# Optimization experiments

Hardware: AMD Instinct MI355X
Metric: run time of the kernel (lower is better)

## Reference

```python
import jax, jax.numpy as jnp
import numpy as np

# ---- dims (match init_kwargs) ----
D_MODEL = 512
N_HEADS = 8
EXPAND = 2
SHRINK = 1
BATCH = 8
SEQ = 4096            # == tno_max_l
DPB_DIM = 512         # dpb_embedding
D1 = EXPAND * D_MODEL                 # 1024 (u_proj / o1 out)
D2 = D_MODEL // SHRINK                # 512  (v_proj out)
HEAD_DIM = D2 // N_HEADS              # 64
EPS = 1e-8


def _srms(x, d):
    # SimpleRMSNorm: x / (||x||_2 * d^-0.5 + eps)
    norm = jnp.linalg.norm(x, axis=-1, keepdims=True)
    return x / (norm * (d ** -0.5) + EPS)


def _dpb(p, Wp, bp, W1, b1, W2, b2, W3, b3):
    # dynamic position bias MLP: scalar rel-pos -> h*head_dim kernel coeffs
    x = p @ Wp + bp
    x = jax.nn.relu(_srms(x, DPB_DIM)) @ W1 + b1
    x = jax.nn.relu(_srms(x, DPB_DIM)) @ W2 + b2
    x = jax.nn.relu(_srms(x, DPB_DIM)) @ W3 + b3
    return x  # (m, h*head_dim)


def _heads(k):
    # (m, h*d) -> (h, m, d)
    return k.reshape(-1, N_HEADS, HEAD_DIM).transpose(1, 0, 2)


def setup_inputs() -> dict:
    key = jax.random.key(0)
    ks = jax.random.split(key, 17)
    w = lambda k, shape: jax.random.normal(k, shape, dtype=jnp.float32) * 0.02
    return {
        "x": jax.random.normal(ks[0], (BATCH, SEQ, D_MODEL), dtype=jnp.float32),
        "Wu": w(ks[1], (D_MODEL, D1)), "bu": w(ks[2], (D1,)),
        "Wv": w(ks[3], (D_MODEL, D2)), "bv": w(ks[4], (D2,)),
        "Wo1": w(ks[5], (D2, D1)), "bo1": w(ks[6], (D1,)),
        "Wo2": w(ks[7], (D1, D_MODEL)), "bo2": w(ks[8], (D_MODEL,)),
        "dpb_Wp": w(ks[9], (1, DPB_DIM)), "dpb_bp": w(ks[10], (DPB_DIM,)),
        "dpb_W1": w(ks[11], (DPB_DIM, DPB_DIM)), "dpb_b1": w(ks[12], (DPB_DIM,)),
        "dpb_W2": w(ks[13], (DPB_DIM, DPB_DIM)), "dpb_b2": w(ks[14], (DPB_DIM,)),
        "dpb_W3": w(ks[15], (DPB_DIM, N_HEADS * HEAD_DIM)),
        "dpb_b3": w(ks[16], (N_HEADS * HEAD_DIM,)),
    }


def reference(x, Wu, bu, Wv, bv, Wo1, bo1, Wo2, bo2,
              dpb_Wp, dpb_bp, dpb_W1, dpb_b1, dpb_W2, dpb_b2, dpb_W3, dpb_b3):
    b, n, _ = x.shape
    shortcut = x
    xn = _srms(x, D2)                                  # pre_norm (SimpleRMSNorm(d2))
    u = jax.nn.silu(xn @ Wu + bu)                      # (b, n, d1)
    v = jax.nn.silu(xn @ Wv + bv)                      # (b, n, d2)
    v = v.reshape(b, n, N_HEADS, HEAD_DIM).transpose(0, 2, 1, 3)  # (b, h, n, d)

    # relative-position indices (par_type=1): 1..n-1, -(n-1)..-1, 0
    pos_idx = jnp.arange(1, n, dtype=jnp.float32)[:, None]   # (n-1, 1)
    neg_idx = -pos_idx[::-1]                                  # (n-1, 1)
    zero_idx = jnp.zeros((1, 1), jnp.float32)
    dpb = lambda p: _dpb(p, dpb_Wp, dpb_bp, dpb_W1, dpb_b1,
                         dpb_W2, dpb_b2, dpb_W3, dpb_b3)
    kz = _heads(dpb(zero_idx))   # (h, 1,   d)
    kp = _heads(dpb(pos_idx))    # (h, n-1, d)
    kn = _heads(dpb(neg_idx))    # (h, n-1, d)
    # circulant embedding of the Toeplitz kernel: [t0, t1..t{n-1}, 0, t{-(n-1)}..t{-1}]
    a = jnp.concatenate([kz, kp, kz, kn], axis=1)             # (h, 2n, d)

    m = 2 * n
    yf = jnp.fft.rfft(v, m, axis=-2)                          # (b, h, n+1, d) complex
    af = jnp.fft.rfft(a, m, axis=-2)[None]                    # (1, h, n+1, d)
    out = jnp.fft.irfft(yf * af, m, axis=-2)[..., :n, :]      # (b, h, n, d)

    out = out.transpose(0, 2, 1, 3).reshape(b, n, D2)         # b n (h d)
    out = (out @ Wo1 + bo1) * u                               # gate
    out = out @ Wo2 + bo2 + shortcut
    return out
```

## Files before the change

### kernel.cpp

```cpp
#include <hip/hip_runtime.h>
#include <hip/hip_fp16.h>


#define FFTN 8192
#define SWZ(p) ((p) ^ (((p) >> 8) & 31))

#define C45F 0.70710678118654752f
#define CC8F 0.92387953251128676f
#define SS8F 0.38268343236508977f

typedef unsigned short u16;
typedef unsigned int u32;
typedef __attribute__((ext_vector_type(8))) short bf16x8;
typedef __attribute__((ext_vector_type(4))) float f32x4;

__device__ __forceinline__ int brev13(int x) { return (int)(__brev((unsigned)x) >> 19); }
__device__ __forceinline__ float b2f(u16 u) {
  union { float f; u32 i; } c; c.i = ((u32)u) << 16; return c.f;
}
__device__ __forceinline__ u16 f2b(float f) {
  union { float f; u32 i; } c; c.f = f;
  u32 r = c.i + 0x7FFFu + ((c.i >> 16) & 1u);
  return (u16)(r >> 16);
}
__device__ __forceinline__ float silu_f(float x) { return x / (1.f + __expf(-x)); }

__device__ __forceinline__ float2 up2(u32 v) {
  __half2 h = __builtin_bit_cast(__half2, v);
  return make_float2(__low2float(h), __high2float(h));
}
__device__ __forceinline__ u32 dn2(float r, float i) {
  __half2 h = __floats2half2_rn(r, i);
  return __builtin_bit_cast(u32, h);
}

__device__ __forceinline__ void gload16(const void* g, void* l) {
  __builtin_amdgcn_global_load_lds(
      (const __attribute__((address_space(1))) u32*)g,
      (__attribute__((address_space(3))) u32*)l, 16, 0, 0);
}

__global__ void twiddle_init_kernel(float2* __restrict__ tw) {
  int k = blockIdx.x * blockDim.x + threadIdx.x;
  if (k < 4096) {
    double ang = -6.283185307179586476925286766559 * ((double)k / 8192.0);
    tw[k] = make_float2((float)cos(ang), (float)sin(ang));
  }
}

__global__ __launch_bounds__(256) void srms_bf16_kernel(
    const float* __restrict__ in, u16* __restrict__ out, int rows, int do_relu)
{
  int wave = threadIdx.x >> 6, lane = threadIdx.x & 63;
  int row = (blockIdx.x << 2) + wave;
  if (row >= rows) return;
  const float4* p = (const float4*)(in + (size_t)row * 512);
  float4 a = p[lane], b = p[lane + 64];
  float ss = a.x*a.x + a.y*a.y + a.z*a.z + a.w*a.w
           + b.x*b.x + b.y*b.y + b.z*b.z + b.w*b.w;
#pragma unroll
  for (int off = 32; off > 0; off >>= 1) ss += __shfl_xor(ss, off);
  float inv = 1.0f / (sqrtf(ss) * 0.04419417382415922f + 1e-8f);
  a.x *= inv; a.y *= inv; a.z *= inv; a.w *= inv;
  b.x *= inv; b.y *= inv; b.z *= inv; b.w *= inv;
  if (do_relu) {
    a.x = fmaxf(a.x, 0.f); a.y = fmaxf(a.y, 0.f); a.z = fmaxf(a.z, 0.f); a.w = fmaxf(a.w, 0.f);
    b.x = fmaxf(b.x, 0.f); b.y = fmaxf(b.y, 0.f); b.z = fmaxf(b.z, 0.f); b.w = fmaxf(b.w, 0.f);
  }
  u16* o = out + (size_t)row * 512;
  ushort4 s0, s1;
  s0.x = f2b(a.x); s0.y = f2b(a.y); s0.z = f2b(a.z); s0.w = f2b(a.w);
  s1.x = f2b(b.x); s1.y = f2b(b.y); s1.z = f2b(b.z); s1.w = f2b(b.w);
  *(ushort4*)(o + lane * 4) = s0;
  *(ushort4*)(o + 256 + lane * 4) = s1;
}

__global__ __launch_bounds__(256) void dpb0_kernel(
    const float* __restrict__ Wp, const float* __restrict__ bp, u16* __restrict__ out)
{
  int wave = threadIdx.x >> 6, lane = threadIdx.x & 63;
  int row = (blockIdx.x << 2) + wave;
  if (row >= 8192) return;
  float pv;
  if (row == 0 || row == 4096) pv = 0.f;
  else if (row < 4096) pv = (float)row;
  else pv = (float)(row - 8192);
  const float4* wp  = (const float4*)Wp;
  const float4* bpp = (const float4*)bp;
  float4 a = wp[lane], b = wp[lane + 64];
  float4 c = bpp[lane], d = bpp[lane + 64];
  a.x = fmaf(pv, a.x, c.x); a.y = fmaf(pv, a.y, c.y);
  a.z = fmaf(pv, a.z, c.z); a.w = fmaf(pv, a.w, c.w);
  b.x = fmaf(pv, b.x, d.x); b.y = fmaf(pv, b.y, d.y);
  b.z = fmaf(pv, b.z, d.z); b.w = fmaf(pv, b.w, d.w);
  float ss = a.x*a.x + a.y*a.y + a.z*a.z + a.w*a.w
           + b.x*b.x + b.y*b.y + b.z*b.z + b.w*b.w;
#pragma unroll
  for (int off = 32; off > 0; off >>= 1) ss += __shfl_xor(ss, off);
  float inv = 1.0f / (sqrtf(ss) * 0.04419417382415922f + 1e-8f);
  u16* o = out + (size_t)row * 512;
  ushort4 s0, s1;
  s0.x = f2b(fmaxf(a.x * inv, 0.f)); s0.y = f2b(fmaxf(a.y * inv, 0.f));
  s0.z = f2b(fmaxf(a.z * inv, 0.f)); s0.w = f2b(fmaxf(a.w * inv, 0.f));
  s1.x = f2b(fmaxf(b.x * inv, 0.f)); s1.y = f2b(fmaxf(b.y * inv, 0.f));
  s1.z = f2b(fmaxf(b.z * inv, 0.f)); s1.w = f2b(fmaxf(b.w * inv, 0.f));
  *(ushort4*)(o + lane * 4) = s0;
  *(ushort4*)(o + 256 + lane * 4) = s1;
}

__global__ __launch_bounds__(256) void wtrans_kernel(
    const float* __restrict__ in, u16* __restrict__ out, int R, int C)
{
  __shared__ float tile[32][33];
  const int c0 = blockIdx.x << 5, r0 = blockIdx.y << 5;
  const int tx = threadIdx.x, ty = threadIdx.y;
#pragma unroll
  for (int i = 0; i < 32; i += 8)
    tile[ty + i][tx] = in[(size_t)(r0 + ty + i) * C + c0 + tx];
  __syncthreads();
#pragma unroll
  for (int i = 0; i < 32; i += 8)
    out[(size_t)(c0 + ty + i) * R + r0 + tx] = f2b(tile[tx][ty + i]);
}

__global__ __launch_bounds__(256) void transpose_b16_kernel(
    const u16* __restrict__ in, u16* __restrict__ out)
{
  __shared__ u16 tile[32][33];
  const int b = blockIdx.z;
  const int j0 = blockIdx.x << 5, c0 = blockIdx.y << 5;
  const int tx = threadIdx.x, ty = threadIdx.y;
  const u16* ip = in + ((size_t)b << 21);
  u16* op = out + ((size_t)b << 21);
#pragma unroll
  for (int i = 0; i < 32; i += 8)
    tile[ty + i][tx] = ip[(size_t)(c0 + ty + i) * 4096 + j0 + tx];
  __syncthreads();
#pragma unroll
  for (int i = 0; i < 32; i += 8)
    op[(size_t)(j0 + ty + i) * 512 + c0 + tx] = tile[tx][ty + i];
}

template <int EPI>
__global__ __launch_bounds__(256) void gemm_bf16_kernel(
    const u16* __restrict__ A, const u16* __restrict__ Bt,
    const float* __restrict__ bias, const u16* __restrict__ aux16,
    const float* __restrict__ auxf, void* __restrict__ Cv,
    int M, int N, int K)
{
  __shared__ __align__(16) u16 As[4096];
  __shared__ __align__(16) u16 Bs[4096];
  const int tid = threadIdx.x;
  const int lane = tid & 63;
  const int w = tid >> 6;
  const int wm = (w >> 1) << 6;
  const int wn = (w & 1) << 6;
  const int lm = lane & 15;
  const int lq = lane >> 4;
  const int bm = blockIdx.y << 7;
  const int bn = blockIdx.x << 7;

  const int sm = tid & 127;
  const int sk = tid >> 7;
  const u16* Ap = A + (size_t)(bm + sm) * K + sk * 8;
  const u16* Bp = Bt + (size_t)(bn + sm) * K + sk * 8;
  u16* As0 = As + ((sk)     * 128 + sm) * 8;
  u16* As1 = As + ((2 + sk) * 128 + sm) * 8;
  u16* Bs0 = Bs + ((sk)     * 128 + sm) * 8;
  u16* Bs1 = Bs + ((2 + sk) * 128 + sm) * 8;

  f32x4 acc[4][4];
#pragma unroll
  for (int i = 0; i < 4; i++)
#pragma unroll
    for (int j = 0; j < 4; j++) acc[i][j] = (f32x4){0.f, 0.f, 0.f, 0.f};

  for (int k0 = 0; k0 < K; k0 += 32) {
    __syncthreads();
    gload16(Ap, As0); gload16(Ap + 16, As1);
    gload16(Bp, Bs0); gload16(Bp + 16, Bs1);
    Ap += 32; Bp += 32;
    __builtin_amdgcn_s_waitcnt(0);
    __syncthreads();
    bf16x8 af[4], bfr[4];
#pragma unroll
    for (int i = 0; i < 4; i++) {
      af[i]  = *(const bf16x8*)(As + (lq * 128 + wm + i * 16 + lm) * 8);
      bfr[i] = *(const bf16x8*)(Bs + (lq * 128 + wn + i * 16 + lm) * 8);
    }
#pragma unroll
    for (int i = 0; i < 4; i++)
#pragma unroll
      for (int j = 0; j < 4; j++)
        acc[i][j] = __builtin_amdgcn_mfma_f32_16x16x32_bf16(af[i], bfr[j], acc[i][j], 0, 0, 0);
  }

#pragma unroll
  for (int i = 0; i < 4; i++) {
    const int m0 = bm + wm + i * 16 + lq * 4;
#pragma unroll
    for (int j = 0; j < 4; j++) {
      const int n = bn + wn + j * 16 + lm;
      const float bb = bias[n];
      const f32x4 v = acc[i][j];
      if constexpr (EPI == 2) {
        const int b = m0 >> 12;
        const int jq = m0 & 4095;
        ushort4 s;
        s.x = f2b(silu_f(v[0] + bb)); s.y = f2b(silu_f(v[1] + bb));
        s.z = f2b(silu_f(v[2] + bb)); s.w = f2b(silu_f(v[3] + bb));
        *(ushort4*)((u16*)Cv + (((size_t)(b * 512 + n)) << 12) + jq) = s;
      } else if constexpr (EPI == 5) {
        float4 o = make_float4(v[0] + bb, v[1] + bb, v[2] + bb, v[3] + bb);
        *(float4*)((float*)Cv + (size_t)n * M + m0) = o;
      } else {
#pragma unroll
        for (int r = 0; r < 4; r++) {
          const size_t idx = (size_t)(m0 + r) * N + n;
          const float val = v[r] + bb;
          if constexpr (EPI == 0) ((float*)Cv)[idx] = val;
          if constexpr (EPI == 1) ((u16*)Cv)[idx] = f2b(silu_f(val));
          if constexpr (EPI == 3) ((u16*)Cv)[idx] = f2b(val * b2f(aux16[idx]));
          if constexpr (EPI == 4) ((float*)Cv)[idx] = val + auxf[idx];
        }
      }
    }
  }
}

__device__ __forceinline__ void fft8192_dit(float* sr, float* si,
                                            const float2* __restrict__ tw)
{
  const int t = threadIdx.x;
  for (int s = 0; s < 12; s += 2) {
    __syncthreads();
    const int h = 1 << s;
#pragma unroll
    for (int bb = 0; bb < 4; bb++) {
      const int u = t + (bb << 9);
      const int j = u & (h - 1);
      const int base = ((u >> s) << (s + 2)) | j;
      const float2 w1 = tw[j << (12 - s)];
      const float2 w2 = tw[j << (11 - s)];
      const int q0 = SWZ(base), q1 = SWZ(base + h);
      const int q2 = SWZ(base + 2 * h), q3 = SWZ(base + 3 * h);
      const float ar = sr[q0], ai = si[q0];
      const float br = sr[q1], bi = si[q1];
      const float cr = sr[q2], ci = si[q2];
      const float dr = sr[q3], di = si[q3];
      const float t1r = br * w1.x - bi * w1.y, t1i = br * w1.y + bi * w1.x;
      const float t2r = dr * w1.x - di * w1.y, t2i = dr * w1.y + di * w1.x;
      const float Ar = ar + t1r, Ai = ai + t1i;
      const float Br = ar - t1r, Bi = ai - t1i;
      const float Cr = cr + t2r, Ci = ci + t2i;
      const float Dr = cr - t2r, Di = ci - t2i;
      const float t3r = Cr * w2.x - Ci * w2.y, t3i = Cr * w2.y + Ci * w2.x;
      const float pr  = Dr * w2.x - Di * w2.y, pi  = Dr * w2.y + Di * w2.x;
      const float t4r = pi, t4i = -pr;
      sr[q0] = Ar + t3r; si[q0] = Ai + t3i;
      sr[q2] = Ar - t3r; si[q2] = Ai - t3i;
      sr[q1] = Br + t4r; si[q1] = Bi + t4i;
      sr[q3] = Br - t4r; si[q3] = Bi - t4i;
    }
  }
  __syncthreads();
#pragma unroll
  for (int bb = 0; bb < 8; bb++) {
    const int u = t + (bb << 9);
    const float2 w = tw[u];
    const int p0 = SWZ(u), p1 = SWZ(u + 4096);
    const float br = sr[p1], bi = si[p1];
    const float trr = br * w.x - bi * w.y;
    const float tri = br * w.y + bi * w.x;
    const float ar = sr[p0], ai = si[p0];
    sr[p0] = ar + trr; si[p0] = ai + tri;
    sr[p1] = ar - trr; si[p1] = ai - tri;
  }
  __syncthreads();
}

__global__ __launch_bounds__(512) void kfft_kernel(
    const float* __restrict__ D1T,
    const float2* __restrict__ tw,
    float2* __restrict__ aspec)
{
  __shared__ float sr[FFTN];
  __shared__ float si[FFTN];
  const int q = blockIdx.x;
  const int t = threadIdx.x;
  const float* row0 = D1T + ((size_t)(2 * q)) * 8192;
  const float* row1 = row0 + 8192;
#pragma unroll
  for (int it = 0; it < 16; it++) {
    const int r = t + (it << 9);
    const int d = SWZ(brev13(r));
    sr[d] = row0[r]; si[d] = row1[r];
  }
  fft8192_dit(sr, si, tw);
  const float sc = 1.0f / 8192.0f;
  float2* O0 = aspec + (size_t)(2 * q) * 4097;
  float2* O1 = aspec + (size_t)(2 * q + 1) * 4097;
#pragma unroll 1
  for (int it = 0; it < 8; it++) {
    const int k = t + (it << 9);
    const int k2 = (FFTN - k) & (FFTN - 1);
    const float zr = sr[SWZ(k)],  zi = si[SWZ(k)];
    const float wr = sr[SWZ(k2)], wi = si[SWZ(k2)];
    O0[k] = make_float2(0.5f * sc * (zr + wr), 0.5f * sc * (zi - wi));
    O1[k] = make_float2(0.5f * sc * (zi + wi), 0.5f * sc * (wr - zr));
  }
  if (t == 0) {
    const float zr = sr[SWZ(4096)], zi = si[SWZ(4096)];
    O0[4096] = make_float2(zr * sc, 0.f);
    O1[4096] = make_float2(zi * sc, 0.f);
  }
}


__device__ __forceinline__ void dit16(float* xr, float* xi,
    float wAr, float wAi, float wBr, float wBi,
    float wCr, float wCi, float wDr, float wDi)
{
#define DITP(a, b, wr_, wi_)                                     \
  { const float cr_ = xr[b]*(wr_) - xi[b]*(wi_);                 \
    const float ci_ = xr[b]*(wi_) + xi[b]*(wr_);                 \
    xr[b] = xr[a] - cr_; xi[b] = xi[a] - ci_;                    \
    xr[a] = xr[a] + cr_; xi[a] = xi[a] + ci_; }
#define DITPM(a, b, wr_, wi_)                                    \
  { const float cr_ = xr[b]*(wr_) - xi[b]*(wi_);                 \
    const float ci_ = xr[b]*(wi_) + xi[b]*(wr_);                 \
    xr[b] = xr[a] - ci_; xi[b] = xi[a] + cr_;                    \
    xr[a] = xr[a] + ci_; xi[a] = xi[a] - cr_; }
  DITP(0,1,wAr,wAi)   DITP(2,3,wAr,wAi)   DITP(4,5,wAr,wAi)   DITP(6,7,wAr,wAi)
  DITP(8,9,wAr,wAi)   DITP(10,11,wAr,wAi) DITP(12,13,wAr,wAi) DITP(14,15,wAr,wAi)
  DITP(0,2,wBr,wBi)   DITPM(1,3,wBr,wBi)
  DITP(4,6,wBr,wBi)   DITPM(5,7,wBr,wBi)
  DITP(8,10,wBr,wBi)  DITPM(9,11,wBr,wBi)
  DITP(12,14,wBr,wBi) DITPM(13,15,wBr,wBi)
  const float wC1r = C45F*(wCr + wCi), wC1i = C45F*(wCi - wCr);
  DITP(0,4,wCr,wCi)   DITP(1,5,wC1r,wC1i)   DITPM(2,6,wCr,wCi)   DITPM(3,7,wC1r,wC1i)
  DITP(8,12,wCr,wCi)  DITP(9,13,wC1r,wC1i)  DITPM(10,14,wCr,wCi) DITPM(11,15,wC1r,wC1i)
  const float wD1r = wDr*CC8F + wDi*SS8F, wD1i = wDi*CC8F - wDr*SS8F;
  const float wD2r = C45F*(wDr + wDi),    wD2i = C45F*(wDi - wDr);
  const float wD3r = wDr*SS8F + wDi*CC8F, wD3i = wDi*SS8F - wDr*CC8F;
  DITP(0,8,wDr,wDi)    DITP(1,9,wD1r,wD1i)   DITP(2,10,wD2r,wD2i)  DITP(3,11,wD3r,wD3i)
  DITPM(4,12,wDr,wDi)  DITPM(5,13,wD1r,wD1i) DITPM(6,14,wD2r,wD2i) DITPM(7,15,wD3r,wD3i)
#undef DITP
#undef DITPM
}

__device__ __forceinline__ void dif16(float* xr, float* xi,
    float wAr, float wAi, float wBr, float wBi,
    float wCr, float wCi, float wDr, float wDi)
{
#define DIFP(a, b, wr_, wi_)                                     \
  { const float dr_ = xr[a] - xr[b], di_ = xi[a] - xi[b];        \
    xr[a] = xr[a] + xr[b]; xi[a] = xi[a] + xi[b];                \
    xr[b] = dr_*(wr_) + di_*(wi_);                               \
    xi[b] = di_*(wr_) - dr_*(wi_); }
#define DIFPM(a, b, wr_, wi_)                                    \
  { const float dr_ = xr[a] - xr[b], di_ = xi[a] - xi[b];        \
    xr[a] = xr[a] + xr[b]; xi[a] = xi[a] + xi[b];                \
    const float er_ = dr_*(wr_) + di_*(wi_);                     \
    const float ei_ = di_*(wr_) - dr_*(wi_);                     \
    xr[b] = -ei_; xi[b] = er_; }
  const float wC1r = C45F*(wCr + wCi), wC1i = C45F*(wCi - wCr);
  const float wD1r = wDr*CC8F + wDi*SS8F, wD1i = wDi*CC8F - wDr*SS8F;
  const float wD2r = C45F*(wDr + wDi),    wD2i = C45F*(wDi - wDr);
  const float wD3r = wDr*SS8F + wDi*CC8F, wD3i = wDi*SS8F - wDr*CC8F;
  DIFP(0,8,wDr,wDi)    DIFP(1,9,wD1r,wD1i)   DIFP(2,10,wD2r,wD2i)  DIFP(3,11,wD3r,wD3i)
  DIFPM(4,12,wDr,wDi)  DIFPM(5,13,wD1r,wD1i) DIFPM(6,14,wD2r,wD2i) DIFPM(7,15,wD3r,wD3i)
  DIFP(0,4,wCr,wCi)   DIFP(1,5,wC1r,wC1i)   DIFPM(2,6,wCr,wCi)   DIFPM(3,7,wC1r,wC1i)
  DIFP(8,12,wCr,wCi)  DIFP(9,13,wC1r,wC1i)  DIFPM(10,14,wCr,wCi) DIFPM(11,15,wC1r,wC1i)
  DIFP(0,2,wBr,wBi)   DIFPM(1,3,wBr,wBi)
  DIFP(4,6,wBr,wBi)   DIFPM(5,7,wBr,wBi)
  DIFP(8,10,wBr,wBi)  DIFPM(9,11,wBr,wBi)
  DIFP(12,14,wBr,wBi) DIFPM(13,15,wBr,wBi)
  DIFP(0,1,wAr,wAi)   DIFP(2,3,wAr,wAi)   DIFP(4,5,wAr,wAi)   DIFP(6,7,wAr,wAi)
  DIFP(8,9,wAr,wAi)   DIFP(10,11,wAr,wAi) DIFP(12,13,wAr,wAi) DIFP(14,15,wAr,wAi)
#undef DIFP
#undef DIFPM
}

template <int SS>
__device__ __forceinline__ void fwd_pass(u32* S, const float2* __restrict__ tw, int u)
{
  const int j = u & ((1 << SS) - 1);
  const int base = ((u >> SS) << (SS + 4)) | j;
  float xr[16], xi[16];
#pragma unroll
  for (int r = 0; r < 16; r++) {
    const float2 v = up2(S[SWZ(base + (r << SS))]);
    xr[r] = v.x; xi[r] = v.y;
  }
  const float2 wA = tw[j << (12 - SS)];
  const float2 wB = tw[j << (11 - SS)];
  const float2 wC = tw[j << (10 - SS)];
  const float2 wD = tw[j << (9 - SS)];
  dit16(xr, xi, wA.x, wA.y, wB.x, wB.y, wC.x, wC.y, wD.x, wD.y);
#pragma unroll
  for (int r = 0; r < 16; r++)
    S[SWZ(base + (r << SS))] = dn2(xr[r], xi[r]);
}

template <int SS>
__device__ __forceinline__ void inv_pass(u32* S, const float2* __restrict__ tw, int u)
{
  const int j = u & ((1 << SS) - 1);
  const int base = ((u >> SS) << (SS + 4)) | j;
  float xr[16], xi[16];
#pragma unroll
  for (int r = 0; r < 16; r++) {
    const float2 v = up2(S[SWZ(base + (r << SS))]);
    xr[r] = v.x; xi[r] = v.y;
  }
  const float2 wA = tw[j << (12 - SS)];
  const float2 wB = tw[j << (11 - SS)];
  const float2 wC = tw[j << (10 - SS)];
  const float2 wD = tw[j << (9 - SS)];
  dif16(xr, xi, wA.x, wA.y, wB.x, wB.y, wC.x, wC.y, wD.x, wD.y);
#pragma unroll
  for (int r = 0; r < 16; r++)
    S[SWZ(base + (r << SS))] = dn2(xr[r], xi[r]);
}

__device__ __forceinline__ void mp2(float zr, float zi, float wr, float wi,
                                    float2 a0, float2 a1,
                                    float& okr, float& oki, float& o2r, float& o2i)
{
  const float Xr = 0.5f*(zr + wr), Xi = 0.5f*(zi - wi);
  const float Yr = 0.5f*(zi + wi), Yi = 0.5f*(wr - zr);
  const float Pr = Xr*a0.x - Xi*a0.y, Pi = Xr*a0.y + Xi*a0.x;
  const float Qr = Yr*a1.x - Yi*a1.y, Qi = Yr*a1.y + Yi*a1.x;
  okr = Pr - Qi; oki = Pi + Qr;
  o2r = Pr + Qi; o2i = Qr - Pi;
}

__global__ __launch_bounds__(512, 4) void conv_kernel(
    const u16* __restrict__ vT,
    const float2* __restrict__ aspec,
    const float2* __restrict__ tw,
    u16* __restrict__ outT)
{
  __shared__ u32 S[FFTN];
  const int q = blockIdx.x;
  const int b = blockIdx.y;
  const int c0 = 2 * q, c1 = 2 * q + 1;
  const int t = threadIdx.x;
  const int db = (int)(__brev((u32)t) >> 23) << 4;

  {
    const u16* p0 = vT + ((size_t)b * 512 + c0) * 4096;
    const u16* p1 = vT + ((size_t)b * 512 + c1) * 4096;
    float xr[16], xi[16];
#pragma unroll
    for (int it = 0; it < 8; it++) {
      const int r = ((it & 1) << 3) | ((it & 2) << 1) | ((it & 4) >> 1);
      const int jg = t + (it << 9);
      xr[r] = b2f(p0[jg]); xi[r] = b2f(p1[jg]);
    }
#pragma unroll
    for (int m = 0; m < 8; m++) { xr[2*m+1] = 0.f; xi[2*m+1] = 0.f; }
    dit16(xr, xi, 1.f, 0.f, 1.f, 0.f, 1.f, 0.f, 1.f, 0.f);
#pragma unroll
    for (int r = 0; r < 16; r++) S[SWZ(db + r)] = dn2(xr[r], xi[r]);
  }
  __syncthreads();
  fwd_pass<4>(S, tw, ((t & 15) << 5) | (t >> 4));
  __syncthreads();
  fwd_pass<8>(S, tw, t);
  __syncthreads();
  {
    const float2* A0 = aspec + (size_t)c0 * 4097;
    const float2* A1 = aspec + (size_t)c1 * 4097;
#pragma unroll
    for (int it = 0; it < 4; it++) {
      const int p = t + (it << 9);
      if (it == 0 && t == 0) {
        const int sA = SWZ(0), sB = SWZ(4096), sC = SWZ(2048), sD = SWZ(6144);
        const float2 a = up2(S[sA]), bb = up2(S[sB]);
        const float Z0r = a.x + bb.x, Z0i = a.y + bb.y;
        const float Z4r = a.x - bb.x, Z4i = a.y - bb.y;
        float N0r, N0i, N4r, N4i, u0, u1;
        mp2(Z0r, Z0i, Z0r, Z0i, A0[0], A1[0], N0r, N0i, u0, u1);
        mp2(Z4r, Z4i, Z4r, Z4i, A0[4096], A1[4096], N4r, N4i, u0, u1);
        S[sA] = dn2(N0r + N4r, N0i + N4i);
        S[sB] = dn2(N0r - N4r, N0i - N4i);
        const float2 c = up2(S[sC]), e = up2(S[sD]);
        const float2 w2 = tw[2048];
        const float trr = e.x*w2.x - e.y*w2.y, tri = e.x*w2.y + e.y*w2.x;
        const float Z2r = c.x + trr, Z2i = c.y + tri;
        const float Z6r = c.x - trr, Z6i = c.y - tri;
        float N2r, N2i, N6r, N6i;
        mp2(Z2r, Z2i, Z6r, Z6i, A0[2048], A1[2048], N2r, N2i, N6r, N6i);
        const float ddr = N2r - N6r, ddi = N2i - N6i;
        S[sC] = dn2(N2r + N6r, N2i + N6i);
        S[sD] = dn2(ddr*w2.x + ddi*w2.y, ddi*w2.x - ddr*w2.y);
      } else {
        const int p2 = 4096 - p;
        const int s0a = SWZ(p),  s1a = SWZ(p + 4096);
        const int s2a = SWZ(p2), s3a = SWZ(p2 + 4096);
        const float2 a1v = up2(S[s0a]), b1v = up2(S[s1a]);
        const float2 a2v = up2(S[s2a]), b2v = up2(S[s3a]);
        const float2 w1 = tw[p], w2 = tw[p2];
        const float t1r = b1v.x*w1.x - b1v.y*w1.y, t1i = b1v.x*w1.y + b1v.y*w1.x;
        const float Zpr = a1v.x + t1r, Zpi = a1v.y + t1i;
        const float Z4r = a1v.x - t1r, Z4i = a1v.y - t1i;
        const float t2r = b2v.x*w2.x - b2v.y*w2.y, t2i = b2v.x*w2.y + b2v.y*w2.x;
        const float Zqr = a2v.x + t2r, Zqi = a2v.y + t2i;
        const float Z8r = a2v.x - t2r, Z8i = a2v.y - t2i;
        float Npr, Npi, N8r, N8i, Nqr, Nqi, N4r, N4i;
        mp2(Zpr, Zpi, Z8r, Z8i, A0[p],  A1[p],  Npr, Npi, N8r, N8i);
        mp2(Zqr, Zqi, Z4r, Z4i, A0[p2], A1[p2], Nqr, Nqi, N4r, N4i);
        float dr = Npr - N4r, di = Npi - N4i;
        S[s0a] = dn2(Npr + N4r, Npi + N4i);
        S[s1a] = dn2(dr*w1.x + di*w1.y, di*w1.x - dr*w1.y);
        dr = Nqr - N8r; di = Nqi - N8i;
        S[s2a] = dn2(Nqr + N8r, Nqi + N8i);
        S[s3a] = dn2(dr*w2.x + di*w2.y, di*w2.x - dr*w2.y);
      }
    }
  }
  __syncthreads();
  inv_pass<8>(S, tw, t);
  __syncthreads();
  inv_pass<4>(S, tw, ((t & 15) << 5) | (t >> 4));
  __syncthreads();
  {
    float xr[16], xi[16];
#pragma unroll
    for (int r = 0; r < 16; r++) {
      const float2 v = up2(S[SWZ(db + r)]);
      xr[r] = v.x; xi[r] = v.y;
    }
    dif16(xr, xi, 1.f, 0.f, 1.f, 0.f, 1.f, 0.f, 1.f, 0.f);
    u16* o0 = outT + ((size_t)b * 512 + c0) * 4096;
    u16* o1 = outT + ((size_t)b * 512 + c1) * 4096;
#pragma unroll
    for (int m = 0; m < 8; m++) {
      const int r = 2 * m;
      const int rv = ((r & 2) << 1) | ((r & 4) >> 1) | ((r & 8) >> 3);
      const int i = t + (rv << 9);
      o0[i] = f2b(xr[r]); o1[i] = f2b(xi[r]);
    }
  }
}

extern "C" void kernel_launch(void* const* d_in, const int* in_sizes, int n_in,
                              void* d_out, int out_size, void* d_ws, size_t ws_size,
                              hipStream_t stream)
{
  const float* x   = (const float*)d_in[0];
  const float* Wu  = (const float*)d_in[1];
  const float* bu  = (const float*)d_in[2];
  const float* Wv  = (const float*)d_in[3];
  const float* bv  = (const float*)d_in[4];
  const float* Wo1 = (const float*)d_in[5];
  const float* bo1 = (const float*)d_in[6];
  const float* Wo2 = (const float*)d_in[7];
  const float* bo2 = (const float*)d_in[8];
  const float* dWp = (const float*)d_in[9];
  const float* dbp = (const float*)d_in[10];
  const float* dW1 = (const float*)d_in[11];
  const float* db1 = (const float*)d_in[12];
  const float* dW2 = (const float*)d_in[13];
  const float* db2 = (const float*)d_in[14];
  const float* dW3 = (const float*)d_in[15];
  const float* db3 = (const float*)d_in[16];
  float* out = (float*)d_out;

  char* wsb = (char*)d_ws;
  const size_t MB = 1u << 20;
  u16* WuT  = (u16*)wsb;
  u16* WvT  = WuT + 524288;
  u16* Wo1T = WvT + 262144;
  u16* Wo2T = Wo1T + 524288;
  u16* dW1T = Wo2T + 524288;
  u16* dW2T = dW1T + 262144;
  u16* dW3T = dW2T + 262144;
  u16*    XNb   = (u16*)(wsb + 6 * MB);
  u16*    D0b   = (u16*)(wsb + 6 * MB);
  float*  D1    = (float*)(wsb + 14 * MB);
  float*  D1T   = (float*)(wsb + 14 * MB);
  u16*    CT    = (u16*)(wsb + 6 * MB);
  u16*    G     = (u16*)(wsb + 6 * MB);
  u16*    VTb   = (u16*)(wsb + 38 * MB);
  float2* ASPEC = (float2*)(wsb + 70 * MB);
  float2* TW    = (float2*)(wsb + 87 * MB);
  u16*    CR    = (u16*)(wsb + 88 * MB);
  u16*    U     = (u16*)(wsb + 128 * MB);

  dim3 wt_blk(32, 8);
  wtrans_kernel<<<dim3(32, 16), wt_blk, 0, stream>>>(Wu, WuT, 512, 1024);
  wtrans_kernel<<<dim3(16, 16), wt_blk, 0, stream>>>(Wv, WvT, 512, 512);
  wtrans_kernel<<<dim3(32, 16), wt_blk, 0, stream>>>(Wo1, Wo1T, 512, 1024);
  wtrans_kernel<<<dim3(16, 32), wt_blk, 0, stream>>>(Wo2, Wo2T, 1024, 512);
  wtrans_kernel<<<dim3(16, 16), wt_blk, 0, stream>>>(dW1, dW1T, 512, 512);
  wtrans_kernel<<<dim3(16, 16), wt_blk, 0, stream>>>(dW2, dW2T, 512, 512);
  wtrans_kernel<<<dim3(16, 16), wt_blk, 0, stream>>>(dW3, dW3T, 512, 512);
  twiddle_init_kernel<<<8, 512, 0, stream>>>(TW);

  srms_bf16_kernel<<<8192, 256, 0, stream>>>(x, XNb, 32768, 0);
  gemm_bf16_kernel<2><<<dim3(4, 256), 256, 0, stream>>>(XNb, WvT, bv, nullptr, nullptr, VTb, 32768, 512, 512);
  gemm_bf16_kernel<1><<<dim3(8, 256), 256, 0, stream>>>(XNb, WuT, bu, nullptr, nullptr, U, 32768, 1024, 512);

  dpb0_kernel<<<2048, 256, 0, stream>>>(dWp, dbp, D0b);
  gemm_bf16_kernel<0><<<dim3(4, 64), 256, 0, stream>>>(D0b, dW1T, db1, nullptr, nullptr, D1, 8192, 512, 512);
  srms_bf16_kernel<<<2048, 256, 0, stream>>>(D1, D0b, 8192, 1);
  gemm_bf16_kernel<0><<<dim3(4, 64), 256, 0, stream>>>(D0b, dW2T, db2, nullptr, nullptr, D1, 8192, 512, 512);
  srms_bf16_kernel<<<2048, 256, 0, stream>>>(D1, D0b, 8192, 1);
  gemm_bf16_kernel<5><<<dim3(4, 64), 256, 0, stream>>>(D0b, dW3T, db3, nullptr, nullptr, D1T, 8192, 512, 512);
  kfft_kernel<<<256, 512, 0, stream>>>(D1T, TW, ASPEC);
  conv_kernel<<<dim3(256, 8), 512, 0, stream>>>(VTb, ASPEC, TW, CT);
  transpose_b16_kernel<<<dim3(128, 16, 8), wt_blk, 0, stream>>>(CT, CR);
  gemm_bf16_kernel<3><<<dim3(8, 256), 256, 0, stream>>>(CR, Wo1T, bo1, U, nullptr, G, 32768, 1024, 512);
  gemm_bf16_kernel<4><<<dim3(4, 256), 256, 0, stream>>>(G, Wo2T, bo2, nullptr, x, out, 32768, 512, 1024);
}
```

Baseline: 682.7 us.

## Double-buffer LDS tiles in bf16 GEMM to overlap global loads with MFMA

Gives the bf16 GEMM two LDS buffers for the A and B tiles. While MFMAs run on one buffer, direct-to-LDS global loads fill the other, using a partial vmcnt wait in place of a full drain. This is meant to hide global memory latency behind compute in the projection GEMMs, at the cost of twice the LDS per block (32 KB), which may reduce occupancy.

```diff
diff --git a/kernel.cpp b/kernel.cpp
--- a/kernel.cpp
+++ b/kernel.cpp
@@ -148,8 +148,8 @@
     const float* __restrict__ auxf, void* __restrict__ Cv,
     int M, int N, int K)
 {
-  __shared__ __align__(16) u16 As[4096];
-  __shared__ __align__(16) u16 Bs[4096];
+  __shared__ __align__(16) u16 As[2][4096];
+  __shared__ __align__(16) u16 Bs[2][4096];
   const int tid = threadIdx.x;
   const int lane = tid & 63;
   const int w = tid >> 6;
@@ -164,10 +164,10 @@
   const int sk = tid >> 7;
   const u16* Ap = A + (size_t)(bm + sm) * K + sk * 8;
   const u16* Bp = Bt + (size_t)(bn + sm) * K + sk * 8;
-  u16* As0 = As + ((sk)     * 128 + sm) * 8;
-  u16* As1 = As + ((2 + sk) * 128 + sm) * 8;
-  u16* Bs0 = Bs + ((sk)     * 128 + sm) * 8;
-  u16* Bs1 = Bs + ((2 + sk) * 128 + sm) * 8;
+  const int so0 = ((sk)     * 128 + sm) * 8;
+  const int so1 = ((2 + sk) * 128 + sm) * 8;
+  const int fo  = (lq * 128 + wm) * 8;
+  const int go  = (lq * 128 + wn) * 8;
 
   f32x4 acc[4][4];
 #pragma unroll
@@ -175,25 +175,53 @@
 #pragma unroll
     for (int j = 0; j < 4; j++) acc[i][j] = (f32x4){0.f, 0.f, 0.f, 0.f};
 
-  for (int k0 = 0; k0 < K; k0 += 32) {
-    __syncthreads();
-    gload16(Ap, As0); gload16(Ap + 16, As1);
-    gload16(Bp, Bs0); gload16(Bp + 16, Bs1);
-    Ap += 32; Bp += 32;
-    __builtin_amdgcn_s_waitcnt(0);
-    __syncthreads();
-    bf16x8 af[4], bfr[4];
-#pragma unroll
-    for (int i = 0; i < 4; i++) {
-      af[i]  = *(const bf16x8*)(As + (lq * 128 + wm + i * 16 + lm) * 8);
-      bfr[i] = *(const bf16x8*)(Bs + (lq * 128 + wn + i * 16 + lm) * 8);
-    }
-#pragma unroll
-    for (int i = 0; i < 4; i++)
-#pragma unroll
-      for (int j = 0; j < 4; j++)
-        acc[i][j] = __builtin_amdgcn_mfma_f32_16x16x32_bf16(af[i], bfr[j], acc[i][j], 0, 0, 0);
-  }
+#define STAGE(buf)                                                  \
+  do {                                                              \
+    gload16(Ap,      &As[buf][0] + so0);                            \
+    gload16(Ap + 16, &As[buf][0] + so1);                            \
+    gload16(Bp,      &Bs[buf][0] + so0);                            \
+    gload16(Bp + 16, &Bs[buf][0] + so1);                            \
+    Ap += 32; Bp += 32;                                             \
+  } while (0)
+
+#define COMPUTE(buf)                                                \
+  do {                                                              \
+    const u16* cA = &As[buf][0];                                    \
+    const u16* cB = &Bs[buf][0];                                    \
+    bf16x8 af[4], bfr[4];                                           \
+    _Pragma("unroll")                                               \
+    for (int i = 0; i < 4; i++) {                                   \
+      af[i]  = *(const bf16x8*)(cA + fo + (i * 16 + lm) * 8);       \
+      bfr[i] = *(const bf16x8*)(cB + go + (i * 16 + lm) * 8);       \
+    }                                                               \
+    _Pragma("unroll")                                               \
+    for (int i = 0; i < 4; i++)                                     \
+      _Pragma("unroll")                                             \
+      for (int j = 0; j < 4; j++)                                   \
+        acc[i][j] = __builtin_amdgcn_mfma_f32_16x16x32_bf16(        \
+            af[i], bfr[j], acc[i][j], 0, 0, 0);                     \
+  } while (0)
+
+  STAGE(0);
+  int cur = 0;
+  for (int k0 = 0; k0 < K - 32; k0 += 32) {
+    if (cur == 0) STAGE(1); else STAGE(0);
+    asm volatile("s_waitcnt vmcnt(4)" ::: "memory");
+    __builtin_amdgcn_sched_barrier(0);
+    __builtin_amdgcn_s_barrier();
+    COMPUTE(cur);
+    asm volatile("s_waitcnt lgkmcnt(0)" ::: "memory");
+    __builtin_amdgcn_sched_barrier(0);
+    __builtin_amdgcn_s_barrier();
+    cur ^= 1;
+  }
+  asm volatile("s_waitcnt vmcnt(0)" ::: "memory");
+  __builtin_amdgcn_sched_barrier(0);
+  __builtin_amdgcn_s_barrier();
+  COMPUTE(cur);
+
+#undef STAGE
+#undef COMPUTE
 
 #pragma unroll
   for (int i = 0; i < 4; i++) {
```

Result: no change. 688.8 us (+0.9%).

## Add 256x256-tile double-buffered bf16 GEMM kernel for large projections

Applied to the files above, without the earlier changes.

Introduces a new GEMM kernel with 256x256 output tiles, 512 threads, double-buffered LDS staging via direct global-to-LDS loads, interleaved B prefetch across quarter-steps, and s_setprio around MFMA bursts. The four large 32768-row GEMMs (u/v projections, gate, output) switch to it, while the small DPB GEMMs keep the old 128x128 kernel. Larger tiles raise operand reuse and cut global traffic per FLOP. The cost is heavy register and LDS use at one block per CU, and fewer blocks in the grid (256 to 512), which may leave wave slots idle.

```diff
diff --git a/kernel.cpp b/kernel.cpp
--- a/kernel.cpp
+++ b/kernel.cpp
@@ -203,6 +203,125 @@
       const int n = bn + wn + j * 16 + lm;
       const float bb = bias[n];
       const f32x4 v = acc[i][j];
+      if constexpr (EPI == 5) {
+        float4 o = make_float4(v[0] + bb, v[1] + bb, v[2] + bb, v[3] + bb);
+        *(float4*)((float*)Cv + (size_t)n * M + m0) = o;
+      } else {
+#pragma unroll
+        for (int r = 0; r < 4; r++) {
+          const size_t idx = (size_t)(m0 + r) * N + n;
+          const float val = v[r] + bb;
+          if constexpr (EPI == 0) ((float*)Cv)[idx] = val;
+          if constexpr (EPI == 1) ((u16*)Cv)[idx] = f2b(silu_f(val));
+          if constexpr (EPI == 3) ((u16*)Cv)[idx] = f2b(val * b2f(aux16[idx]));
+          if constexpr (EPI == 4) ((float*)Cv)[idx] = val + auxf[idx];
+        }
+      }
+    }
+  }
+}
+
+template <int EPI>
+__global__ __launch_bounds__(512, 1) void gemm256_bf16_kernel(
+    const u16* __restrict__ A, const u16* __restrict__ Bt,
+    const float* __restrict__ bias, const u16* __restrict__ aux16,
+    const float* __restrict__ auxf, void* __restrict__ Cv,
+    int M, int N, int K)
+{
+  __shared__ __align__(16) u16 Asm[2][16384];
+  __shared__ __align__(16) u16 Bsm[2][16384];
+  const int tid = threadIdx.x;
+  const int lane = tid & 63;
+  const int w = tid >> 6;
+  const int wm = (w >> 2) << 7;
+  const int wn = (w & 3) << 6;
+  const int lm = lane & 15;
+  const int lq = lane >> 4;
+  const int bm = blockIdx.y << 8;
+  const int bn = blockIdx.x << 8;
+
+  const int rloc = tid & 127;
+  const int kq0 = tid >> 7;
+  const u16* Ag = A + (size_t)(bm + rloc) * K + kq0 * 8;
+  const u16* Bg = Bt + (size_t)(bn + rloc) * K + kq0 * 8;
+  const size_t hstep = (size_t)128 * K;
+  const int lso = tid * 8;
+
+  const int aBase = ((wm >> 7) * 8192) + lq * 1024 + lm * 8;
+
+  f32x4 acc[8][4];
+#pragma unroll
+  for (int i = 0; i < 8; i++)
+#pragma unroll
+    for (int j = 0; j < 4; j++) acc[i][j] = (f32x4){0.f, 0.f, 0.f, 0.f};
+
+#define STG256(gb, lb, hh, kt) do {                                       \
+    const u16* g_ = (gb) + (size_t)(hh) * hstep + (size_t)(kt) * 64;      \
+    u16* l_ = (lb) + (hh) * 8192 + lso;                                   \
+    gload16(g_, l_); gload16(g_ + 32, l_ + 4096);                         \
+  } while (0)
+
+  STG256(Ag, &Asm[0][0], 0, 0); STG256(Ag, &Asm[0][0], 1, 0);
+  STG256(Bg, &Bsm[0][0], 0, 0); STG256(Bg, &Bsm[0][0], 1, 0);
+
+  const int NT = K >> 6;
+  for (int t = 0; t < NT; ++t) {
+    const int cb = t & 1, nb = cb ^ 1;
+    const u16* cA = &Asm[cb][0];
+    const u16* cB = &Bsm[cb][0];
+    if (t + 1 < NT) {
+      STG256(Ag, &Asm[nb][0], 0, t + 1);
+      STG256(Ag, &Asm[nb][0], 1, t + 1);
+      asm volatile("s_waitcnt vmcnt(4)" ::: "memory");
+    } else {
+      asm volatile("s_waitcnt vmcnt(0)" ::: "memory");
+    }
+    __builtin_amdgcn_s_barrier();
+    bf16x8 af[4][2];
+#pragma unroll
+    for (int q = 0; q < 4; ++q) {
+      const int qm = q >> 1, qn = q & 1;
+      if (q == 0 && t + 1 < NT) STG256(Bg, &Bsm[nb][0], 0, t + 1);
+      if (q == 1 && t + 1 < NT) STG256(Bg, &Bsm[nb][0], 1, t + 1);
+      if (qn == 0) {
+#pragma unroll
+        for (int i = 0; i < 4; ++i)
+#pragma unroll
+          for (int ks = 0; ks < 2; ++ks)
+            af[i][ks] = *(const bf16x8*)(cA + aBase + ks * 4096 + qm * 512 + i * 128);
+      }
+      const int colBase = wn + qn * 32;
+      const int bBase = ((colBase >> 7) * 8192) + lq * 1024 + (colBase & 127) * 8 + lm * 8;
+      bf16x8 bfr[2][2];
+#pragma unroll
+      for (int j = 0; j < 2; ++j)
+#pragma unroll
+        for (int ks = 0; ks < 2; ++ks)
+          bfr[j][ks] = *(const bf16x8*)(cB + bBase + ks * 4096 + j * 128);
+      __builtin_amdgcn_s_setprio(1);
+#pragma unroll
+      for (int i = 0; i < 4; ++i)
+#pragma unroll
+        for (int j = 0; j < 2; ++j) {
+          acc[qm*4+i][qn*2+j] = __builtin_amdgcn_mfma_f32_16x16x32_bf16(
+              af[i][0], bfr[j][0], acc[qm*4+i][qn*2+j], 0, 0, 0);
+          acc[qm*4+i][qn*2+j] = __builtin_amdgcn_mfma_f32_16x16x32_bf16(
+              af[i][1], bfr[j][1], acc[qm*4+i][qn*2+j], 0, 0, 0);
+        }
+      __builtin_amdgcn_s_setprio(0);
+      __builtin_amdgcn_s_barrier();
+    }
+  }
+#undef STG256
+
+#pragma unroll
+  for (int im = 0; im < 8; im++) {
+    const int m0 = bm + wm + im * 16 + lq * 4;
+#pragma unroll
+    for (int jn = 0; jn < 4; jn++) {
+      const int n = bn + wn + jn * 16 + lm;
+      const float bb = bias[n];
+      const f32x4 v = acc[im][jn];
       if constexpr (EPI == 2) {
         const int b = m0 >> 12;
         const int jq = m0 & 4095;
@@ -210,15 +329,11 @@
         s.x = f2b(silu_f(v[0] + bb)); s.y = f2b(silu_f(v[1] + bb));
         s.z = f2b(silu_f(v[2] + bb)); s.w = f2b(silu_f(v[3] + bb));
         *(ushort4*)((u16*)Cv + (((size_t)(b * 512 + n)) << 12) + jq) = s;
-      } else if constexpr (EPI == 5) {
-        float4 o = make_float4(v[0] + bb, v[1] + bb, v[2] + bb, v[3] + bb);
-        *(float4*)((float*)Cv + (size_t)n * M + m0) = o;
       } else {
 #pragma unroll
         for (int r = 0; r < 4; r++) {
           const size_t idx = (size_t)(m0 + r) * N + n;
           const float val = v[r] + bb;
-          if constexpr (EPI == 0) ((float*)Cv)[idx] = val;
           if constexpr (EPI == 1) ((u16*)Cv)[idx] = f2b(silu_f(val));
           if constexpr (EPI == 3) ((u16*)Cv)[idx] = f2b(val * b2f(aux16[idx]));
           if constexpr (EPI == 4) ((float*)Cv)[idx] = val + auxf[idx];
@@ -601,8 +716,8 @@
   twiddle_init_kernel<<<8, 512, 0, stream>>>(TW);
 
   srms_bf16_kernel<<<8192, 256, 0, stream>>>(x, XNb, 32768, 0);
-  gemm_bf16_kernel<2><<<dim3(4, 256), 256, 0, stream>>>(XNb, WvT, bv, nullptr, nullptr, VTb, 32768, 512, 512);
-  gemm_bf16_kernel<1><<<dim3(8, 256), 256, 0, stream>>>(XNb, WuT, bu, nullptr, nullptr, U, 32768, 1024, 512);
+  gemm256_bf16_kernel<2><<<dim3(2, 128), 512, 0, stream>>>(XNb, WvT, bv, nullptr, nullptr, VTb, 32768, 512, 512);
+  gemm256_bf16_kernel<1><<<dim3(4, 128), 512, 0, stream>>>(XNb, WuT, bu, nullptr, nullptr, U, 32768, 1024, 512);
 
   dpb0_kernel<<<2048, 256, 0, stream>>>(dWp, dbp, D0b);
   gemm_bf16_kernel<0><<<dim3(4, 64), 256, 0, stream>>>(D0b, dW1T, db1, nullptr, nullptr, D1, 8192, 512, 512);
@@ -613,6 +728,6 @@
   kfft_kernel<<<256, 512, 0, stream>>>(D1T, TW, ASPEC);
   conv_kernel<<<dim3(256, 8), 512, 0, stream>>>(VTb, ASPEC, TW, CT);
   transpose_b16_kernel<<<dim3(128, 16, 8), wt_blk, 0, stream>>>(CT, CR);
-  gemm_bf16_kernel<3><<<dim3(8, 256), 256, 0, stream>>>(CR, Wo1T, bo1, U, nullptr, G, 32768, 1024, 512);
-  gemm_bf16_kernel<4><<<dim3(4, 256), 256, 0, stream>>>(G, Wo2T, bo2, nullptr, x, out, 32768, 512, 1024);
-}
+  gemm256_bf16_kernel<3><<<dim3(4, 128), 512, 0, stream>>>(CR, Wo1T, bo1, U, nullptr, G, 32768, 1024, 512);
+  gemm256_bf16_kernel<4><<<dim3(2, 128), 512, 0, stream>>>(G, Wo2T, bo2, nullptr, x, out, 32768, 512, 1024);
+}
```

New measurement: 652.9 us. -4.4%, faster.
